# Performance work log

Hardware: AMD Instinct MI355X
Metric: run time of the kernel (lower is better)

The kernel has to match this reference:

```python
import jax, jax.numpy as jnp
import numpy as np

KERNELSIZE = 9


def generate_pe(pos_num, d_num):
    pos = jnp.arange(pos_num, dtype=jnp.float32)[:, None]
    d_i = jnp.arange(0, d_num + 1, 2, dtype=jnp.float32)[None, :]
    ang = pos / jnp.power(jnp.float32(10000.0), d_i / d_num)  # [pos, ceil((d+1)/2)]
    pe = jnp.zeros((pos_num, d_num), dtype=jnp.float32)
    n_even = pe[:, 0::2].shape[1]
    n_odd = pe[:, 1::2].shape[1]
    pe = pe.at[:, 0::2].set(jnp.sin(ang)[:, :n_even])
    pe = pe.at[:, 1::2].set(jnp.cos(ang)[:, :n_odd])
    return pe


def nearest_idx(in_size, out_size):
    # torch F.interpolate(mode='nearest'): src = floor(dst * in/out)
    return jnp.floor(jnp.arange(out_size) * (in_size / out_size)).astype(jnp.int32)


def setup_inputs() -> dict:
    N, K, C_in, C_out, ks = 30000, 16, 256, 128, KERNELSIZE
    key = jax.random.key(0)
    k0, k1, k2, k3, k4, k5, k6, k7 = jax.random.split(key, 8)
    return {
        "ndata": jax.random.normal(k0, (N, C_in), jnp.float32),
        "neighbors": jax.random.randint(k1, (N, K), 0, N),
        "W_lin": jax.random.normal(k2, (C_out, C_in), jnp.float32) * 0.05,
        "b_lin": jax.random.normal(k3, (C_out,), jnp.float32) * 0.05,
        "weight": jax.random.normal(k4, (C_out, ks), jnp.float32),
        "bias": jax.random.normal(k5, (C_out,), jnp.float32),
        "W_res": jax.random.normal(k6, (C_out, C_in), jnp.float32) * 0.05,
        "b_res": jax.random.normal(k7, (C_out,), jnp.float32) * 0.05,
    }


def reference(ndata, neighbors, W_lin, b_lin, weight, bias, W_res, b_res):
    N = ndata.shape[0]
    C_out, ks = weight.shape
    feat = ndata @ W_lin.T + b_lin                              # [N, D]
    # mailbox = in-neighbor features + self-loop (dgl.add_self_loop)
    mailbox = jnp.concatenate([feat[neighbors], feat[:, None, :]], axis=1)  # [N, S, D]
    S = mailbox.shape[1]
    x = jnp.sort(mailbox, axis=1)                                # sort along neighbor dim
    idx = nearest_idx(ks, S)
    pe = generate_pe(ks, C_out)                                  # [ks, D]
    x = x + pe[idx][None, :, :]                                  # interpolated PE
    w_local = weight[:, idx].T                                   # [S, D] interpolated weight
    Xf = jnp.fft.fft(x, axis=1)
    Wf = jnp.fft.fft(w_local, axis=0)
    y = jnp.fft.ifft(Xf * jnp.conj(Wf)[None, :, :], axis=1).real  # circular correlation
    h = y.sum(axis=1) + bias                                     # [N, D]
    return h + ndata @ W_res.T + b_res
```

## Files before the change

kernel.cpp:

```cpp
#include <hip/hip_runtime.h>
#include <math.h>

#define N_NODES 30000
#define K_NBR   16
#define C_IN    256
#define C_OUT   128
#define KS      9
#define S_MB    17
#define BR      32

typedef __attribute__((ext_vector_type(4))) float f32x4;
typedef __attribute__((ext_vector_type(2))) float f32x2;
typedef __attribute__((ext_vector_type(8))) short bf16x8;

static __device__ __forceinline__ ushort f2bf(float f) {
    uint u = __builtin_bit_cast(uint, f);
    u += 0x7fffu + ((u >> 16) & 1u);
    return (ushort)(u >> 16);
}

__global__ __launch_bounds__(256)
void pcg_prep(const float* __restrict__ W_lin,
              const float* __restrict__ W_res,
              const float* __restrict__ weight,
              const float* __restrict__ b_lin,
              const float* __restrict__ bias,
              const float* __restrict__ b_res,
              ushort* __restrict__ Bf,
              float* __restrict__ Ws,
              float* __restrict__ Cd) {
    if (blockIdx.x == 32) {
        int d = threadIdx.x;
        if (d >= C_OUT) return;
        float freq = powf(10000.0f, -(float)(d & ~1) / (float)C_OUT);
        float ws = 0.f, p = 0.f;
        for (int s = 0; s < S_MB; ++s) {
            int idx = (int)floorf((float)s * (9.0f / 17.0f));
            ws += weight[d * KS + idx];
            float ang = (float)idx * freq;
            p += (d & 1) ? cosf(ang) : sinf(ang);
        }
        Ws[d] = ws;
        Cd[d] = ws * ((float)(K_NBR + 1) * b_lin[d] + p) + bias[d] + b_res[d];
        return;
    }
    const int tt     = blockIdx.x * 256 + threadIdx.x;
    const int col_lo = tt & 15;
    const int ksub   = (tt >> 4) & 3;
    const int colhi  = (tt >> 6) & 15;
    const int kc     = tt >> 10;
    const int col    = colhi * 16 + col_lo;
    const int k0     = kc * 32 + ksub * 8;
    const float* Wr = (col < C_OUT)
        ? &W_lin[(size_t)col * C_IN + k0]
        : &W_res[(size_t)(col - C_OUT) * C_IN + k0];
    const f32x4 w0 = *reinterpret_cast<const f32x4*>(Wr);
    const f32x4 w1 = *reinterpret_cast<const f32x4*>(Wr + 4);
    ushort b[8] = { f2bf(w0.x), f2bf(w0.y), f2bf(w0.z), f2bf(w0.w),
                    f2bf(w1.x), f2bf(w1.y), f2bf(w1.z), f2bf(w1.w) };
    *reinterpret_cast<uint4*>(&Bf[(size_t)tt * 8]) =
        *reinterpret_cast<const uint4*>(b);
}

__global__ __launch_bounds__(512, 8)
void pcg_mfma(const float* __restrict__ ndata,
              const ushort* __restrict__ Bf,
              const float* __restrict__ Ws,
              const float* __restrict__ Cd,
              ushort* __restrict__ Gs,
              ushort* __restrict__ Pc) {
    __shared__ short sA[8192];

    const int t  = threadIdx.x;
    const int n0 = blockIdx.x * BR;

#pragma unroll
    for (int i = 0; i < 2; ++i) {
        const int v    = i * 512 + t;
        const int row  = v >> 5;
        const int kch  = v & 31;
        f32x4 a0 = {0.f, 0.f, 0.f, 0.f}, a1 = {0.f, 0.f, 0.f, 0.f};
        if (n0 + row < N_NODES) {
            const float* p = &ndata[(size_t)(n0 + row) * C_IN + kch * 8];
            a0 = *reinterpret_cast<const f32x4*>(p);
            a1 = *reinterpret_cast<const f32x4*>(p + 4);
        }
        const int kc   = kch >> 2;
        const int ksub = kch & 3;
        const int f    = kc * 2 + (row >> 4);
        const int up   = (((row & 15) | (ksub << 4)) ^ ksub) ^ ((kc & 1) << 2);
        uint4 w;
        w.x = (uint)f2bf(a0.x) | ((uint)f2bf(a0.y) << 16);
        w.y = (uint)f2bf(a0.z) | ((uint)f2bf(a0.w) << 16);
        w.z = (uint)f2bf(a1.x) | ((uint)f2bf(a1.y) << 16);
        w.w = (uint)f2bf(a1.z) | ((uint)f2bf(a1.w) << 16);
        *reinterpret_cast<uint4*>(&sA[f * 512 + up * 8]) = w;
    }
    __syncthreads();

    const int wave = t >> 6;
    const int l    = t & 63;
    const int bu   = l ^ (l >> 4);

    const int chG = wave;
    const int chR = 8 + wave;

    f32x4 acc[2][2] = {};

#pragma unroll
    for (int kc = 0; kc < 8; ++kc) {
        const int ux = bu ^ ((kc & 1) << 2);
        bf16x8 a[2];
#pragma unroll
        for (int rg = 0; rg < 2; ++rg)
            a[rg] = *reinterpret_cast<const bf16x8*>(
                        &sA[(kc * 2 + rg) * 512 + ux * 8]);
        bf16x8 bG = *reinterpret_cast<const bf16x8*>(
                        &Bf[((size_t)(kc * 16 + chG) * 64 + l) * 8]);
        bf16x8 bR = *reinterpret_cast<const bf16x8*>(
                        &Bf[((size_t)(kc * 16 + chR) * 64 + l) * 8]);
#pragma unroll
        for (int rg = 0; rg < 2; ++rg) {
            acc[rg][0] = __builtin_amdgcn_mfma_f32_16x16x32_bf16(
                             a[rg], bG, acc[rg][0], 0, 0, 0);
            acc[rg][1] = __builtin_amdgcn_mfma_f32_16x16x32_bf16(
                             a[rg], bR, acc[rg][1], 0, 0, 0);
        }
    }

    const int c   = wave * 16 + (l & 15);
    const float wsc = Ws[c];
    const float cdc = Cd[c];
    const int rl  = (l >> 4) * 4;
#pragma unroll
    for (int rg = 0; rg < 2; ++rg) {
#pragma unroll
        for (int j = 0; j < 4; ++j) {
            const int row = n0 + rg * 16 + rl + j;
            if (row < N_NODES) {
                const float gs = wsc * acc[rg][0][j];
                Gs[(size_t)row * C_OUT + c] = f2bf(gs);
                Pc[(size_t)row * C_OUT + c] = f2bf(gs + acc[rg][1][j] + cdc);
            }
        }
    }
}

__global__ __launch_bounds__(256)
void pcg_gather(const int* __restrict__ neighbors,
                const ushort* __restrict__ Gs,
                const ushort* __restrict__ Pc,
                float* __restrict__ out) {
    __shared__ int snb[64];
    const int t = threadIdx.x;
    if (t < 64) snb[t] = neighbors[(size_t)blockIdx.x * 64 + t];
    __syncthreads();

    const int g = t >> 6;
    const int l = t & 63;
    const int n = blockIdx.x * 4 + g;

    uint p = *reinterpret_cast<const uint*>(&Pc[(size_t)n * C_OUT + 2 * l]);
    float a0 = __builtin_bit_cast(float, p << 16);
    float a1 = __builtin_bit_cast(float, p & 0xffff0000u);

#pragma unroll
    for (int k = 0; k < K_NBR; ++k) {
        const int m = snb[g * 16 + k];
        uint v = *reinterpret_cast<const uint*>(&Gs[(size_t)m * C_OUT + 2 * l]);
        a0 += __builtin_bit_cast(float, v << 16);
        a1 += __builtin_bit_cast(float, v & 0xffff0000u);
    }

    f32x2 o = {a0, a1};
    *reinterpret_cast<f32x2*>(&out[(size_t)n * C_OUT + 2 * l]) = o;
}

extern "C" void kernel_launch(void* const* d_in, const int* in_sizes, int n_in,
                              void* d_out, int out_size, void* d_ws, size_t ws_size,
                              hipStream_t stream) {
    const float* ndata     = (const float*)d_in[0];
    const int*   neighbors = (const int*)  d_in[1];
    const float* W_lin     = (const float*)d_in[2];
    const float* b_lin     = (const float*)d_in[3];
    const float* weight    = (const float*)d_in[4];
    const float* bias      = (const float*)d_in[5];
    const float* W_res     = (const float*)d_in[6];
    const float* b_res     = (const float*)d_in[7];
    float* out = (float*)d_out;

    ushort* Bf = (ushort*)d_ws;
    ushort* Gq = Bf + 65536;
    ushort* Pq = Gq + (size_t)N_NODES * C_OUT;
    float*  Ws = (float*)(Pq + (size_t)N_NODES * C_OUT);
    float*  Cd = Ws + C_OUT;

    pcg_prep<<<33, 256, 0, stream>>>(W_lin, W_res, weight, b_lin, bias, b_res,
                                     Bf, Ws, Cd);
    pcg_mfma<<<(N_NODES + BR - 1) / BR, 512, 0, stream>>>(
        ndata, Bf, Ws, Cd, Gq, Pq);
    pcg_gather<<<N_NODES / 4, 256, 0, stream>>>(neighbors, Gq, Pq, out);
}
```

Baseline: 40.18 us.

## Process two row tiles per block with double-buffered LDS to overlap loads

Each GEMM block now handles two 32-row tiles, using two LDS buffers so the global load of the second tile's ndata is issued before computing the first tile. This aims to hide global memory latency behind MFMA work and halves the grid size. In exchange LDS per block doubles, occupancy hint drops to 4 blocks per CU, and fewer blocks are launched, which may reduce latency hiding across waves.

```diff
diff --git a/kernel.cpp b/kernel.cpp
--- a/kernel.cpp
+++ b/kernel.cpp
@@ -8,6 +8,7 @@
 #define KS      9
 #define S_MB    17
 #define BR      32
+#define NT      938
 
 typedef __attribute__((ext_vector_type(4))) float f32x4;
 typedef __attribute__((ext_vector_type(2))) float f32x2;
@@ -62,88 +63,120 @@
         *reinterpret_cast<const uint4*>(b);
 }
 
-__global__ __launch_bounds__(512, 8)
+__global__ __launch_bounds__(512, 4)
 void pcg_mfma(const float* __restrict__ ndata,
               const ushort* __restrict__ Bf,
               const float* __restrict__ Ws,
               const float* __restrict__ Cd,
               ushort* __restrict__ Gs,
               ushort* __restrict__ Pc) {
-    __shared__ short sA[8192];
-
-    const int t  = threadIdx.x;
-    const int n0 = blockIdx.x * BR;
-
-#pragma unroll
-    for (int i = 0; i < 2; ++i) {
-        const int v    = i * 512 + t;
-        const int row  = v >> 5;
-        const int kch  = v & 31;
-        f32x4 a0 = {0.f, 0.f, 0.f, 0.f}, a1 = {0.f, 0.f, 0.f, 0.f};
-        if (n0 + row < N_NODES) {
-            const float* p = &ndata[(size_t)(n0 + row) * C_IN + kch * 8];
-            a0 = *reinterpret_cast<const f32x4*>(p);
-            a1 = *reinterpret_cast<const f32x4*>(p + 4);
-        }
-        const int kc   = kch >> 2;
-        const int ksub = kch & 3;
-        const int f    = kc * 2 + (row >> 4);
-        const int up   = (((row & 15) | (ksub << 4)) ^ ksub) ^ ((kc & 1) << 2);
-        uint4 w;
-        w.x = (uint)f2bf(a0.x) | ((uint)f2bf(a0.y) << 16);
-        w.y = (uint)f2bf(a0.z) | ((uint)f2bf(a0.w) << 16);
-        w.z = (uint)f2bf(a1.x) | ((uint)f2bf(a1.y) << 16);
-        w.w = (uint)f2bf(a1.z) | ((uint)f2bf(a1.w) << 16);
-        *reinterpret_cast<uint4*>(&sA[f * 512 + up * 8]) = w;
-    }
-    __syncthreads();
-
+    __shared__ short sA0[8192];
+    __shared__ short sA1[8192];
+
+    const int t    = threadIdx.x;
     const int wave = t >> 6;
     const int l    = t & 63;
     const int bu   = l ^ (l >> 4);
-
-    const int chG = wave;
-    const int chR = 8 + wave;
-
-    f32x4 acc[2][2] = {};
-
-#pragma unroll
-    for (int kc = 0; kc < 8; ++kc) {
-        const int ux = bu ^ ((kc & 1) << 2);
-        bf16x8 a[2];
-#pragma unroll
-        for (int rg = 0; rg < 2; ++rg)
-            a[rg] = *reinterpret_cast<const bf16x8*>(
-                        &sA[(kc * 2 + rg) * 512 + ux * 8]);
-        bf16x8 bG = *reinterpret_cast<const bf16x8*>(
-                        &Bf[((size_t)(kc * 16 + chG) * 64 + l) * 8]);
-        bf16x8 bR = *reinterpret_cast<const bf16x8*>(
-                        &Bf[((size_t)(kc * 16 + chR) * 64 + l) * 8]);
-#pragma unroll
-        for (int rg = 0; rg < 2; ++rg) {
-            acc[rg][0] = __builtin_amdgcn_mfma_f32_16x16x32_bf16(
-                             a[rg], bG, acc[rg][0], 0, 0, 0);
-            acc[rg][1] = __builtin_amdgcn_mfma_f32_16x16x32_bf16(
-                             a[rg], bR, acc[rg][1], 0, 0, 0);
-        }
-    }
-
-    const int c   = wave * 16 + (l & 15);
+    const int chG  = wave;
+    const int chR  = 8 + wave;
+    const int c    = wave * 16 + (l & 15);
+    const int rl   = (l >> 4) * 4;
     const float wsc = Ws[c];
     const float cdc = Cd[c];
-    const int rl  = (l >> 4) * 4;
-#pragma unroll
-    for (int rg = 0; rg < 2; ++rg) {
-#pragma unroll
-        for (int j = 0; j < 4; ++j) {
-            const int row = n0 + rg * 16 + rl + j;
-            if (row < N_NODES) {
-                const float gs = wsc * acc[rg][0][j];
-                Gs[(size_t)row * C_OUT + c] = f2bf(gs);
-                Pc[(size_t)row * C_OUT + c] = f2bf(gs + acc[rg][1][j] + cdc);
-            }
-        }
-    }
+
+    const int tile0 = blockIdx.x * 2;
+
+    const int row0 = t >> 5;
+    const int row1 = (512 + t) >> 5;
+    const int kch  = t & 31;
+    const int kc0  = kch >> 2, ks0 = kch & 3;
+    const int f0   = kc0 * 2 + (row0 >> 4);
+    const int up0  = (((row0 & 15) | (ks0 << 4)) ^ ks0) ^ ((kc0 & 1) << 2);
+    const int f1   = kc0 * 2 + (row1 >> 4);
+    const int up1  = (((row1 & 15) | (ks0 << 4)) ^ ks0) ^ ((kc0 & 1) << 2);
+
+#define STAGE_LOAD(TILE, R0A, R0B, R1A, R1B)                                   \
+    {                                                                          \
+        const int n0_ = (TILE) * BR;                                           \
+        R0A = (f32x4){0.f,0.f,0.f,0.f}; R0B = R0A; R1A = R0A; R1B = R0A;       \
+        if (n0_ + row0 < N_NODES) {                                            \
+            const float* p_ = &ndata[(size_t)(n0_ + row0) * C_IN + kch * 8];   \
+            R0A = *reinterpret_cast<const f32x4*>(p_);                         \
+            R0B = *reinterpret_cast<const f32x4*>(p_ + 4);                     \
+        }                                                                      \
+        if (n0_ + row1 < N_NODES) {                                            \
+            const float* p_ = &ndata[(size_t)(n0_ + row1) * C_IN + kch * 8];   \
+            R1A = *reinterpret_cast<const f32x4*>(p_);                         \
+            R1B = *reinterpret_cast<const f32x4*>(p_ + 4);                     \
+        }                                                                      \
+    }
+
+#define STAGE_WRITE(SBUF, R0A, R0B, R1A, R1B)                                  \
+    {                                                                          \
+        uint4 w_;                                                              \
+        w_.x = (uint)f2bf(R0A.x) | ((uint)f2bf(R0A.y) << 16);                  \
+        w_.y = (uint)f2bf(R0A.z) | ((uint)f2bf(R0A.w) << 16);                  \
+        w_.z = (uint)f2bf(R0B.x) | ((uint)f2bf(R0B.y) << 16);                  \
+        w_.w = (uint)f2bf(R0B.z) | ((uint)f2bf(R0B.w) << 16);                  \
+        *reinterpret_cast<uint4*>(&SBUF[f0 * 512 + up0 * 8]) = w_;             \
+        w_.x = (uint)f2bf(R1A.x) | ((uint)f2bf(R1A.y) << 16);                  \
+        w_.y = (uint)f2bf(R1A.z) | ((uint)f2bf(R1A.w) << 16);                  \
+        w_.z = (uint)f2bf(R1B.x) | ((uint)f2bf(R1B.y) << 16);                  \
+        w_.w = (uint)f2bf(R1B.z) | ((uint)f2bf(R1B.w) << 16);                  \
+        *reinterpret_cast<uint4*>(&SBUF[f1 * 512 + up1 * 8]) = w_;             \
+    }
+
+#define COMPUTE_STORE(SBUF, TILE)                                              \
+    {                                                                          \
+        const int n0_ = (TILE) * BR;                                           \
+        f32x4 accG0 = {}, accG1 = {}, accR0 = {}, accR1 = {};                  \
+        _Pragma("unroll")                                                      \
+        for (int kc = 0; kc < 8; ++kc) {                                       \
+            const int ux = bu ^ ((kc & 1) << 2);                               \
+            const bf16x8 a0 = *reinterpret_cast<const bf16x8*>(                \
+                &SBUF[(kc * 2 + 0) * 512 + ux * 8]);                           \
+            const bf16x8 a1 = *reinterpret_cast<const bf16x8*>(                \
+                &SBUF[(kc * 2 + 1) * 512 + ux * 8]);                           \
+            const bf16x8 bG = *reinterpret_cast<const bf16x8*>(                \
+                &Bf[((size_t)(kc * 16 + chG) * 64 + l) * 8]);                  \
+            const bf16x8 bR = *reinterpret_cast<const bf16x8*>(                \
+                &Bf[((size_t)(kc * 16 + chR) * 64 + l) * 8]);                  \
+            accG0 = __builtin_amdgcn_mfma_f32_16x16x32_bf16(a0, bG, accG0, 0, 0, 0); \
+            accR0 = __builtin_amdgcn_mfma_f32_16x16x32_bf16(a0, bR, accR0, 0, 0, 0); \
+            accG1 = __builtin_amdgcn_mfma_f32_16x16x32_bf16(a1, bG, accG1, 0, 0, 0); \
+            accR1 = __builtin_amdgcn_mfma_f32_16x16x32_bf16(a1, bR, accR1, 0, 0, 0); \
+        }                                                                      \
+        _Pragma("unroll")                                                      \
+        for (int j = 0; j < 4; ++j) {                                          \
+            const int r0_ = n0_ + rl + j;                                      \
+            if (r0_ < N_NODES) {                                               \
+                const float g_ = wsc * accG0[j];                               \
+                Gs[(size_t)r0_ * C_OUT + c] = f2bf(g_);                        \
+                Pc[(size_t)r0_ * C_OUT + c] = f2bf(g_ + accR0[j] + cdc);       \
+            }                                                                  \
+            const int r1_ = n0_ + 16 + rl + j;                                 \
+            if (r1_ < N_NODES) {                                               \
+                const float g_ = wsc * accG1[j];                               \
+                Gs[(size_t)r1_ * C_OUT + c] = f2bf(g_);                        \
+                Pc[(size_t)r1_ * C_OUT + c] = f2bf(g_ + accR1[j] + cdc);       \
+            }                                                                  \
+        }                                                                      \
+    }
+
+    f32x4 r0a, r0b, r1a, r1b;
+    STAGE_LOAD(tile0, r0a, r0b, r1a, r1b);
+    STAGE_WRITE(sA0, r0a, r0b, r1a, r1b);
+    __syncthreads();
+
+    STAGE_LOAD(tile0 + 1, r0a, r0b, r1a, r1b);
+    COMPUTE_STORE(sA0, tile0);
+    STAGE_WRITE(sA1, r0a, r0b, r1a, r1b);
+    __syncthreads();
+    COMPUTE_STORE(sA1, tile0 + 1);
+
+#undef STAGE_LOAD
+#undef STAGE_WRITE
+#undef COMPUTE_STORE
 }
 
 __global__ __launch_bounds__(256)
@@ -197,7 +230,6 @@
 
     pcg_prep<<<33, 256, 0, stream>>>(W_lin, W_res, weight, b_lin, bias, b_res,
                                      Bf, Ws, Cd);
-    pcg_mfma<<<(N_NODES + BR - 1) / BR, 512, 0, stream>>>(
-        ndata, Bf, Ws, Cd, Gq, Pq);
+    pcg_mfma<<<NT / 2, 512, 0, stream>>>(ndata, Bf, Ws, Cd, Gq, Pq);
     pcg_gather<<<N_NODES / 4, 256, 0, stream>>>(neighbors, Gq, Pq, out);
 }
```

Result: slower. 41.53 us (+3.4%).
